# Kernel tuning notes

Hardware: AMD Instinct MI355X
Metric: run time of the kernel (lower is better)

## Reference

```python
import jax, jax.numpy as jnp
import numpy as np

NEG_BIG = -1e12
ALPHA = 0.2  # leaky_relu negative slope


def setup_inputs() -> dict:
    key = jax.random.key(0)
    k1, k2, k3, k4, k5 = jax.random.split(key, 5)
    B, N, C_in, C_out = 8, 2048, 128, 128
    x = jax.random.normal(k1, (B, N, C_in), dtype=jnp.float32)
    adj = jax.random.randint(k2, (B, N, N), 0, 2, dtype=jnp.int32)
    W = jax.random.normal(k3, (C_in, C_out), dtype=jnp.float32)
    a = jax.random.normal(k4, (C_out, 2), dtype=jnp.float32)
    bias = jax.random.normal(k5, (C_out,), dtype=jnp.float32)
    return {"x": x, "adj": adj, "W": W, "a": a, "bias": bias}


def reference(x, adj, W, a, bias):
    # hidden: [B, N, C_out]
    hidden = jnp.matmul(x, W)
    # additive attention components: [B, N, 2] -> attn1, attn2 each [B, N]
    scores = jnp.matmul(hidden, a)
    attn1 = scores[..., 0]
    attn2 = scores[..., 1]
    # outer-sum: [B, N, N]
    attn = attn1[:, :, None] + attn2[:, None, :]
    attn = jnp.where(attn >= 0, attn, ALPHA * attn)  # leaky_relu
    attn = attn + jnp.where(adj > 0, 0.0, NEG_BIG)
    attn = jax.nn.softmax(attn, axis=-1)
    # dropout is identity in eval/reference mode
    out = jnp.matmul(attn, hidden) + bias
    return out
```

## Files before the change

kernel.cpp:

```cpp
#include <hip/hip_runtime.h>
#include <hip/hip_bf16.h>

#define ALPHA 0.2f
#define NEG_BIG -1e12f

constexpr int B_ = 8, N_ = 2048, C_ = 128;
constexpr int IB = 32, JB = 64, NJT = N_ / JB;

typedef __attribute__((ext_vector_type(8))) short short8;
typedef __attribute__((ext_vector_type(8))) unsigned short ushort8;
typedef __attribute__((ext_vector_type(4))) float f32x4;

__device__ __forceinline__ unsigned short f2bf(float f) {
    unsigned int u = __float_as_uint(f);
    u += 0x7fffu + ((u >> 16) & 1u);
    return (unsigned short)(u >> 16);
}

__global__ __launch_bounds__(256) void k1_hidden(
    const float* __restrict__ x, const float* __restrict__ W,
    const float* __restrict__ a, unsigned short* __restrict__ hT,
    float* __restrict__ at1, float* __restrict__ at2)
{
    __shared__ float xs[64][C_];
    __shared__ float Ws[C_][C_];
    const int tid = threadIdx.x;
    const int row0 = blockIdx.x * 64;

    {
        const float4* xsrc = (const float4*)(x + (size_t)row0 * C_);
        float4* xdst = (float4*)&xs[0][0];
        for (int i = tid; i < 64 * C_ / 4; i += 256) xdst[i] = xsrc[i];
        const float4* wsrc = (const float4*)W;
        float4* wdst = (float4*)&Ws[0][0];
        for (int i = tid; i < C_ * C_ / 4; i += 256) wdst[i] = wsrc[i];
    }
    __syncthreads();

    const int tr = tid >> 5, tc = tid & 31;
    const int r0 = tr * 8, c0 = tc * 4;

    float acc[8][4];
#pragma unroll
    for (int i = 0; i < 8; ++i)
#pragma unroll
        for (int j = 0; j < 4; ++j) acc[i][j] = 0.f;

    for (int k = 0; k < C_; k += 4) {
        float4 w0 = *(const float4*)&Ws[k + 0][c0];
        float4 w1 = *(const float4*)&Ws[k + 1][c0];
        float4 w2 = *(const float4*)&Ws[k + 2][c0];
        float4 w3 = *(const float4*)&Ws[k + 3][c0];
#pragma unroll
        for (int rr = 0; rr < 8; ++rr) {
            float4 xv = *(const float4*)&xs[r0 + rr][k];
            acc[rr][0] += xv.x * w0.x + xv.y * w1.x + xv.z * w2.x + xv.w * w3.x;
            acc[rr][1] += xv.x * w0.y + xv.y * w1.y + xv.z * w2.y + xv.w * w3.y;
            acc[rr][2] += xv.x * w0.z + xv.y * w1.z + xv.z * w2.z + xv.w * w3.z;
            acc[rr][3] += xv.x * w0.w + xv.y * w1.w + xv.z * w2.w + xv.w * w3.w;
        }
    }

    float av0[4], av1[4];
#pragma unroll
    for (int cc = 0; cc < 4; ++cc) {
        av0[cc] = a[(c0 + cc) * 2 + 0];
        av1[cc] = a[(c0 + cc) * 2 + 1];
    }
#pragma unroll
    for (int rr = 0; rr < 8; ++rr) {
        float s1 = acc[rr][0] * av0[0] + acc[rr][1] * av0[1] +
                   acc[rr][2] * av0[2] + acc[rr][3] * av0[3];
        float s2 = acc[rr][0] * av1[0] + acc[rr][1] * av1[1] +
                   acc[rr][2] * av1[2] + acc[rr][3] * av1[3];
#pragma unroll
        for (int off = 1; off < 32; off <<= 1) {
            s1 += __shfl_xor(s1, off);
            s2 += __shfl_xor(s2, off);
        }
        if (tc == 0) {
            at1[row0 + r0 + rr] = s1;
            at2[row0 + r0 + rr] = s2;
        }
    }

    const int b = row0 >> 11;
    const int n0 = row0 & (N_ - 1);
#pragma unroll
    for (int cc = 0; cc < 4; ++cc) {
        ushort8 hv;
#pragma unroll
        for (int rr = 0; rr < 8; ++rr) hv[rr] = f2bf(acc[rr][cc]);
        *(ushort8*)(hT + ((size_t)b * C_ + c0 + cc) * N_ + n0 + r0) = hv;
    }
}

__global__ __launch_bounds__(256) void k2_attn(
    const int* __restrict__ adj, const unsigned short* __restrict__ hT,
    const float* __restrict__ at1, const float* __restrict__ at2,
    const float* __restrict__ bias, float* __restrict__ out)
{
    __shared__ unsigned short P[IB][JB + 8];
    __shared__ float mrow[IB], lrow[IB], srow[IB];

    const int tid = threadIdx.x;
    const int b = blockIdx.x >> 6;
    const int i0 = (blockIdx.x & 63) * IB;

    const int r = tid >> 3;
    const int jl = tid & 7;

    if (tid < IB) { mrow[tid] = -3e38f; lrow[tid] = 0.f; }
    __syncthreads();

    const float a1 = at1[(size_t)b * N_ + i0 + r];
    const int* arow = adj + ((size_t)b * N_ + i0 + r) * N_ + jl * 8;
    const float* a2p = at2 + (size_t)b * N_ + jl * 8;

    const int lane = tid & 63;
    const int wv = tid >> 6;
    const int lg = lane >> 4;
    const int ll = lane & 15;
    const unsigned short* hb0 = hT + ((size_t)b * C_ + wv * 32 + ll) * N_;
    const unsigned short* hb1 = hb0 + (size_t)16 * N_;

    f32x4 acc00 = {0.f, 0.f, 0.f, 0.f}, acc01 = {0.f, 0.f, 0.f, 0.f};
    f32x4 acc10 = {0.f, 0.f, 0.f, 0.f}, acc11 = {0.f, 0.f, 0.f, 0.f};

    int4 pf0 = *(const int4*)arow;
    int4 pf1 = *(const int4*)(arow + 4);

    for (int jt = 0; jt < NJT; ++jt) {
        int4 A0 = pf0, A1 = pf1;
        if (jt + 1 < NJT) {
            pf0 = *(const int4*)(arow + (jt + 1) * JB);
            pf1 = *(const int4*)(arow + (jt + 1) * JB + 4);
        }
        float4 f0 = *(const float4*)(a2p + jt * JB);
        float4 f1 = *(const float4*)(a2p + jt * JB + 4);

        float s[8];
        {
            float t;
            t = a1 + f0.x; t = t >= 0.f ? t : ALPHA * t; s[0] = A0.x > 0 ? t : t + NEG_BIG;
            t = a1 + f0.y; t = t >= 0.f ? t : ALPHA * t; s[1] = A0.y > 0 ? t : t + NEG_BIG;
            t = a1 + f0.z; t = t >= 0.f ? t : ALPHA * t; s[2] = A0.z > 0 ? t : t + NEG_BIG;
            t = a1 + f0.w; t = t >= 0.f ? t : ALPHA * t; s[3] = A0.w > 0 ? t : t + NEG_BIG;
            t = a1 + f1.x; t = t >= 0.f ? t : ALPHA * t; s[4] = A1.x > 0 ? t : t + NEG_BIG;
            t = a1 + f1.y; t = t >= 0.f ? t : ALPHA * t; s[5] = A1.y > 0 ? t : t + NEG_BIG;
            t = a1 + f1.z; t = t >= 0.f ? t : ALPHA * t; s[6] = A1.z > 0 ? t : t + NEG_BIG;
            t = a1 + f1.w; t = t >= 0.f ? t : ALPHA * t; s[7] = A1.w > 0 ? t : t + NEG_BIG;
        }
        float tm = s[0];
#pragma unroll
        for (int e = 1; e < 8; ++e) tm = fmaxf(tm, s[e]);
        tm = fmaxf(tm, __shfl_xor(tm, 1));
        tm = fmaxf(tm, __shfl_xor(tm, 2));
        tm = fmaxf(tm, __shfl_xor(tm, 4));

        const float m_old = mrow[r];
        const float m_new = fmaxf(m_old, tm);

        float p[8];
        float ps = 0.f;
#pragma unroll
        for (int e = 0; e < 8; ++e) { p[e] = __expf(s[e] - m_new); ps += p[e]; }
        ps += __shfl_xor(ps, 1);
        ps += __shfl_xor(ps, 2);
        ps += __shfl_xor(ps, 4);

        ushort8 pw;
#pragma unroll
        for (int e = 0; e < 8; ++e) pw[e] = f2bf(p[e]);
        *(ushort8*)&P[r][jl * 8] = pw;

        if (jl == 0) {
            const float sc = __expf(m_old - m_new);
            srow[r] = sc;
            mrow[r] = m_new;
            lrow[r] = lrow[r] * sc + ps;
        }
        __syncthreads();

        const char* Pb = (const char*)P;
        short8 pa0 = *(const short8*)(Pb + ll * 144 + lg * 16);
        short8 pa1 = *(const short8*)(Pb + ll * 144 + lg * 16 + 64);
        short8 pa2 = *(const short8*)(Pb + (ll + 16) * 144 + lg * 16);
        short8 pa3 = *(const short8*)(Pb + (ll + 16) * 144 + lg * 16 + 64);

        const unsigned short* hrow0 = hb0 + jt * JB;
        const unsigned short* hrow1 = hb1 + jt * JB;
        short8 vb00 = *(const short8*)(hrow0 + lg * 8);
        short8 vb01 = *(const short8*)(hrow0 + 32 + lg * 8);
        short8 vb10 = *(const short8*)(hrow1 + lg * 8);
        short8 vb11 = *(const short8*)(hrow1 + 32 + lg * 8);

        float4 sc0 = *(const float4*)&srow[lg * 4];
        float4 sc1 = *(const float4*)&srow[16 + lg * 4];
        acc00[0] *= sc0.x; acc00[1] *= sc0.y; acc00[2] *= sc0.z; acc00[3] *= sc0.w;
        acc01[0] *= sc0.x; acc01[1] *= sc0.y; acc01[2] *= sc0.z; acc01[3] *= sc0.w;
        acc10[0] *= sc1.x; acc10[1] *= sc1.y; acc10[2] *= sc1.z; acc10[3] *= sc1.w;
        acc11[0] *= sc1.x; acc11[1] *= sc1.y; acc11[2] *= sc1.z; acc11[3] *= sc1.w;

        acc00 = __builtin_amdgcn_mfma_f32_16x16x32_bf16(pa0, vb00, acc00, 0, 0, 0);
        acc00 = __builtin_amdgcn_mfma_f32_16x16x32_bf16(pa1, vb01, acc00, 0, 0, 0);
        acc01 = __builtin_amdgcn_mfma_f32_16x16x32_bf16(pa0, vb10, acc01, 0, 0, 0);
        acc01 = __builtin_amdgcn_mfma_f32_16x16x32_bf16(pa1, vb11, acc01, 0, 0, 0);
        acc10 = __builtin_amdgcn_mfma_f32_16x16x32_bf16(pa2, vb00, acc10, 0, 0, 0);
        acc10 = __builtin_amdgcn_mfma_f32_16x16x32_bf16(pa3, vb01, acc10, 0, 0, 0);
        acc11 = __builtin_amdgcn_mfma_f32_16x16x32_bf16(pa2, vb10, acc11, 0, 0, 0);
        acc11 = __builtin_amdgcn_mfma_f32_16x16x32_bf16(pa3, vb11, acc11, 0, 0, 0);

        __syncthreads();
    }

    float4 lw0 = *(const float4*)&lrow[lg * 4];
    float4 lw1 = *(const float4*)&lrow[16 + lg * 4];
    const int c = wv * 32 + ll;
    const float bv0 = bias[c];
    const float bv1 = bias[c + 16];

    float* o0 = out + ((size_t)b * N_ + i0 + lg * 4) * C_ + c;
    o0[0 * C_]      = acc00[0] / lw0.x + bv0;
    o0[1 * C_]      = acc00[1] / lw0.y + bv0;
    o0[2 * C_]      = acc00[2] / lw0.z + bv0;
    o0[3 * C_]      = acc00[3] / lw0.w + bv0;
    o0[0 * C_ + 16] = acc01[0] / lw0.x + bv1;
    o0[1 * C_ + 16] = acc01[1] / lw0.y + bv1;
    o0[2 * C_ + 16] = acc01[2] / lw0.z + bv1;
    o0[3 * C_ + 16] = acc01[3] / lw0.w + bv1;

    float* o1 = o0 + (size_t)16 * C_;
    o1[0 * C_]      = acc10[0] / lw1.x + bv0;
    o1[1 * C_]      = acc10[1] / lw1.y + bv0;
    o1[2 * C_]      = acc10[2] / lw1.z + bv0;
    o1[3 * C_]      = acc10[3] / lw1.w + bv0;
    o1[0 * C_ + 16] = acc11[0] / lw1.x + bv1;
    o1[1 * C_ + 16] = acc11[1] / lw1.y + bv1;
    o1[2 * C_ + 16] = acc11[2] / lw1.z + bv1;
    o1[3 * C_ + 16] = acc11[3] / lw1.w + bv1;
}

extern "C" void kernel_launch(void* const* d_in, const int* in_sizes, int n_in,
                              void* d_out, int out_size, void* d_ws, size_t ws_size,
                              hipStream_t stream) {
    const float* x    = (const float*)d_in[0];
    const int*   adj  = (const int*)d_in[1];
    const float* W    = (const float*)d_in[2];
    const float* a    = (const float*)d_in[3];
    const float* bias = (const float*)d_in[4];
    float* out = (float*)d_out;

    char* ws = (char*)d_ws;
    unsigned short* hT = (unsigned short*)ws;
    float* at1 = (float*)(ws + (size_t)4 * 1024 * 1024);
    float* at2 = (float*)(ws + (size_t)4 * 1024 * 1024 + 64 * 1024);

    k1_hidden<<<(B_ * N_) / 64, 256, 0, stream>>>(x, W, a, hT, at1, at2);
    k2_attn<<<B_ * (N_ / IB), 256, 0, stream>>>(adj, hT, at1, at2, bias, out);
}
```

Before: 85.60 us.

## Retile attention kernel to 16x128 with double-buffered P and LDS-staged at2

Changes the attention tile from 32 rows x 64 columns to 16 rows x 128 columns, so the grid doubles and each block runs half as many j-iterations, with more MFMA work per iteration. The P and srow buffers are double-buffered, which removes the trailing barrier in each iteration. The at2 vector is staged in LDS once per block instead of being read from global memory every iteration, and the float-to-bf16 conversion uses the packed v_cvt_pk_bf16_f32 instruction. The cost is that hT is re-read by twice as many blocks, and the launch bound now requests 4 blocks per CU.

Result: no change. 87.08 us (+1.7%).

```diff
diff --git a/kernel.cpp b/kernel.cpp
--- a/kernel.cpp
+++ b/kernel.cpp
@@ -5,7 +5,7 @@
 #define NEG_BIG -1e12f
 
 constexpr int B_ = 8, N_ = 2048, C_ = 128;
-constexpr int IB = 32, JB = 64, NJT = N_ / JB;
+constexpr int IB = 16, JB = 128, NJT = N_ / JB;
 
 typedef __attribute__((ext_vector_type(8))) short short8;
 typedef __attribute__((ext_vector_type(8))) unsigned short ushort8;
@@ -15,6 +15,12 @@
     unsigned int u = __float_as_uint(f);
     u += 0x7fffu + ((u >> 16) & 1u);
     return (unsigned short)(u >> 16);
+}
+
+__device__ __forceinline__ unsigned int cvtpk_bf16(float lo, float hi) {
+    unsigned int r;
+    asm("v_cvt_pk_bf16_f32 %0, %1, %2" : "=v"(r) : "v"(lo), "v"(hi));
+    return r;
 }
 
 __global__ __launch_bounds__(256) void k1_hidden(
@@ -95,68 +101,84 @@
     }
 }
 
-__global__ __launch_bounds__(256) void k2_attn(
+__global__ __launch_bounds__(256, 4) void k2_attn(
     const int* __restrict__ adj, const unsigned short* __restrict__ hT,
     const float* __restrict__ at1, const float* __restrict__ at2,
     const float* __restrict__ bias, float* __restrict__ out)
 {
-    __shared__ unsigned short P[IB][JB + 8];
-    __shared__ float mrow[IB], lrow[IB], srow[IB];
+    __shared__ unsigned short P[2][IB][JB + 8];
+    __shared__ float at2s[N_];
+    __shared__ float mrow[IB], lrow[IB], srow[2][IB];
 
     const int tid = threadIdx.x;
-    const int b = blockIdx.x >> 6;
-    const int i0 = (blockIdx.x & 63) * IB;
-
-    const int r = tid >> 3;
-    const int jl = tid & 7;
-
+    const int b  = blockIdx.x >> 7;
+    const int i0 = (blockIdx.x & 127) * IB;
+
+    {
+        const float4* src = (const float4*)(at2 + (size_t)b * N_);
+        float4* dst = (float4*)at2s;
+        dst[tid]       = src[tid];
+        dst[tid + 256] = src[tid + 256];
+    }
     if (tid < IB) { mrow[tid] = -3e38f; lrow[tid] = 0.f; }
-    __syncthreads();
-
+
+    const int r  = tid >> 4;
+    const int jl = tid & 15;
     const float a1 = at1[(size_t)b * N_ + i0 + r];
-    const int* arow = adj + ((size_t)b * N_ + i0 + r) * N_ + jl * 8;
-    const float* a2p = at2 + (size_t)b * N_ + jl * 8;
+    const int* arow = adj + ((size_t)(b * N_ + i0 + r)) * N_ + jl * 8;
 
     const int lane = tid & 63;
     const int wv = tid >> 6;
     const int lg = lane >> 4;
     const int ll = lane & 15;
-    const unsigned short* hb0 = hT + ((size_t)b * C_ + wv * 32 + ll) * N_;
-    const unsigned short* hb1 = hb0 + (size_t)16 * N_;
-
-    f32x4 acc00 = {0.f, 0.f, 0.f, 0.f}, acc01 = {0.f, 0.f, 0.f, 0.f};
-    f32x4 acc10 = {0.f, 0.f, 0.f, 0.f}, acc11 = {0.f, 0.f, 0.f, 0.f};
+    const unsigned short* hb = hT + ((size_t)b * C_ + wv * 32 + ll) * N_;
+
+    f32x4 acc0 = {0.f, 0.f, 0.f, 0.f}, acc1 = {0.f, 0.f, 0.f, 0.f};
 
     int4 pf0 = *(const int4*)arow;
     int4 pf1 = *(const int4*)(arow + 4);
 
+    __syncthreads();
+
     for (int jt = 0; jt < NJT; ++jt) {
+        const int buf = jt & 1;
+
+        short8 vb0[4], vb1[4];
+        {
+            const unsigned short* hrow = hb + jt * JB + lg * 8;
+#pragma unroll
+            for (int ks = 0; ks < 4; ++ks) {
+                vb0[ks] = *(const short8*)(hrow + ks * 32);
+                vb1[ks] = *(const short8*)(hrow + (size_t)16 * N_ + ks * 32);
+            }
+        }
+
         int4 A0 = pf0, A1 = pf1;
         if (jt + 1 < NJT) {
             pf0 = *(const int4*)(arow + (jt + 1) * JB);
             pf1 = *(const int4*)(arow + (jt + 1) * JB + 4);
         }
-        float4 f0 = *(const float4*)(a2p + jt * JB);
-        float4 f1 = *(const float4*)(a2p + jt * JB + 4);
+        float4 f0 = *(const float4*)&at2s[jt * JB + jl * 8];
+        float4 f1 = *(const float4*)&at2s[jt * JB + jl * 8 + 4];
 
         float s[8];
         {
             float t;
-            t = a1 + f0.x; t = t >= 0.f ? t : ALPHA * t; s[0] = A0.x > 0 ? t : t + NEG_BIG;
-            t = a1 + f0.y; t = t >= 0.f ? t : ALPHA * t; s[1] = A0.y > 0 ? t : t + NEG_BIG;
-            t = a1 + f0.z; t = t >= 0.f ? t : ALPHA * t; s[2] = A0.z > 0 ? t : t + NEG_BIG;
-            t = a1 + f0.w; t = t >= 0.f ? t : ALPHA * t; s[3] = A0.w > 0 ? t : t + NEG_BIG;
-            t = a1 + f1.x; t = t >= 0.f ? t : ALPHA * t; s[4] = A1.x > 0 ? t : t + NEG_BIG;
-            t = a1 + f1.y; t = t >= 0.f ? t : ALPHA * t; s[5] = A1.y > 0 ? t : t + NEG_BIG;
-            t = a1 + f1.z; t = t >= 0.f ? t : ALPHA * t; s[6] = A1.z > 0 ? t : t + NEG_BIG;
-            t = a1 + f1.w; t = t >= 0.f ? t : ALPHA * t; s[7] = A1.w > 0 ? t : t + NEG_BIG;
-        }
-        float tm = s[0];
-#pragma unroll
-        for (int e = 1; e < 8; ++e) tm = fmaxf(tm, s[e]);
+            t = a1 + f0.x; t = fmaxf(t, ALPHA * t); s[0] = A0.x > 0 ? t : NEG_BIG;
+            t = a1 + f0.y; t = fmaxf(t, ALPHA * t); s[1] = A0.y > 0 ? t : NEG_BIG;
+            t = a1 + f0.z; t = fmaxf(t, ALPHA * t); s[2] = A0.z > 0 ? t : NEG_BIG;
+            t = a1 + f0.w; t = fmaxf(t, ALPHA * t); s[3] = A0.w > 0 ? t : NEG_BIG;
+            t = a1 + f1.x; t = fmaxf(t, ALPHA * t); s[4] = A1.x > 0 ? t : NEG_BIG;
+            t = a1 + f1.y; t = fmaxf(t, ALPHA * t); s[5] = A1.y > 0 ? t : NEG_BIG;
+            t = a1 + f1.z; t = fmaxf(t, ALPHA * t); s[6] = A1.z > 0 ? t : NEG_BIG;
+            t = a1 + f1.w; t = fmaxf(t, ALPHA * t); s[7] = A1.w > 0 ? t : NEG_BIG;
+        }
+        float tm = fmaxf(fmaxf(fmaxf(s[0], s[1]), fmaxf(s[2], s[3])),
+                         fmaxf(fmaxf(s[4], s[5]), fmaxf(s[6], s[7])));
         tm = fmaxf(tm, __shfl_xor(tm, 1));
         tm = fmaxf(tm, __shfl_xor(tm, 2));
         tm = fmaxf(tm, __shfl_xor(tm, 4));
+        tm = fmaxf(tm, __shfl_xor(tm, 8));
 
         const float m_old = mrow[r];
         const float m_new = fmaxf(m_old, tm);
@@ -168,77 +190,54 @@
         ps += __shfl_xor(ps, 1);
         ps += __shfl_xor(ps, 2);
         ps += __shfl_xor(ps, 4);
-
-        ushort8 pw;
-#pragma unroll
-        for (int e = 0; e < 8; ++e) pw[e] = f2bf(p[e]);
-        *(ushort8*)&P[r][jl * 8] = pw;
+        ps += __shfl_xor(ps, 8);
+
+        int4 pw;
+        pw.x = (int)cvtpk_bf16(p[0], p[1]);
+        pw.y = (int)cvtpk_bf16(p[2], p[3]);
+        pw.z = (int)cvtpk_bf16(p[4], p[5]);
+        pw.w = (int)cvtpk_bf16(p[6], p[7]);
+        *(int4*)&P[buf][r][jl * 8] = pw;
 
         if (jl == 0) {
             const float sc = __expf(m_old - m_new);
-            srow[r] = sc;
+            srow[buf][r] = sc;
             mrow[r] = m_new;
             lrow[r] = lrow[r] * sc + ps;
         }
         __syncthreads();
 
-        const char* Pb = (const char*)P;
-        short8 pa0 = *(const short8*)(Pb + ll * 144 + lg * 16);
-        short8 pa1 = *(const short8*)(Pb + ll * 144 + lg * 16 + 64);
-        short8 pa2 = *(const short8*)(Pb + (ll + 16) * 144 + lg * 16);
-        short8 pa3 = *(const short8*)(Pb + (ll + 16) * 144 + lg * 16 + 64);
-
-        const unsigned short* hrow0 = hb0 + jt * JB;
-        const unsigned short* hrow1 = hb1 + jt * JB;
-        short8 vb00 = *(const short8*)(hrow0 + lg * 8);
-        short8 vb01 = *(const short8*)(hrow0 + 32 + lg * 8);
-        short8 vb10 = *(const short8*)(hrow1 + lg * 8);
-        short8 vb11 = *(const short8*)(hrow1 + 32 + lg * 8);
-
-        float4 sc0 = *(const float4*)&srow[lg * 4];
-        float4 sc1 = *(const float4*)&srow[16 + lg * 4];
-        acc00[0] *= sc0.x; acc00[1] *= sc0.y; acc00[2] *= sc0.z; acc00[3] *= sc0.w;
-        acc01[0] *= sc0.x; acc01[1] *= sc0.y; acc01[2] *= sc0.z; acc01[3] *= sc0.w;
-        acc10[0] *= sc1.x; acc10[1] *= sc1.y; acc10[2] *= sc1.z; acc10[3] *= sc1.w;
-        acc11[0] *= sc1.x; acc11[1] *= sc1.y; acc11[2] *= sc1.z; acc11[3] *= sc1.w;
-
-        acc00 = __builtin_amdgcn_mfma_f32_16x16x32_bf16(pa0, vb00, acc00, 0, 0, 0);
-        acc00 = __builtin_amdgcn_mfma_f32_16x16x32_bf16(pa1, vb01, acc00, 0, 0, 0);
-        acc01 = __builtin_amdgcn_mfma_f32_16x16x32_bf16(pa0, vb10, acc01, 0, 0, 0);
-        acc01 = __builtin_amdgcn_mfma_f32_16x16x32_bf16(pa1, vb11, acc01, 0, 0, 0);
-        acc10 = __builtin_amdgcn_mfma_f32_16x16x32_bf16(pa2, vb00, acc10, 0, 0, 0);
-        acc10 = __builtin_amdgcn_mfma_f32_16x16x32_bf16(pa3, vb01, acc10, 0, 0, 0);
-        acc11 = __builtin_amdgcn_mfma_f32_16x16x32_bf16(pa2, vb10, acc11, 0, 0, 0);
-        acc11 = __builtin_amdgcn_mfma_f32_16x16x32_bf16(pa3, vb11, acc11, 0, 0, 0);
-
-        __syncthreads();
-    }
-
-    float4 lw0 = *(const float4*)&lrow[lg * 4];
-    float4 lw1 = *(const float4*)&lrow[16 + lg * 4];
+        const char* Pb = (const char*)P[buf];
+        short8 pa[4];
+#pragma unroll
+        for (int ks = 0; ks < 4; ++ks)
+            pa[ks] = *(const short8*)(Pb + ll * 272 + ks * 64 + lg * 16);
+
+        float4 sc4 = *(const float4*)&srow[buf][lg * 4];
+        acc0[0] *= sc4.x; acc0[1] *= sc4.y; acc0[2] *= sc4.z; acc0[3] *= sc4.w;
+        acc1[0] *= sc4.x; acc1[1] *= sc4.y; acc1[2] *= sc4.z; acc1[3] *= sc4.w;
+
+#pragma unroll
+        for (int ks = 0; ks < 4; ++ks) {
+            acc0 = __builtin_amdgcn_mfma_f32_16x16x32_bf16(pa[ks], vb0[ks], acc0, 0, 0, 0);
+            acc1 = __builtin_amdgcn_mfma_f32_16x16x32_bf16(pa[ks], vb1[ks], acc1, 0, 0, 0);
+        }
+    }
+
+    float4 lw = *(const float4*)&lrow[lg * 4];
     const int c = wv * 32 + ll;
     const float bv0 = bias[c];
     const float bv1 = bias[c + 16];
 
-    float* o0 = out + ((size_t)b * N_ + i0 + lg * 4) * C_ + c;
-    o0[0 * C_]      = acc00[0] / lw0.x + bv0;
-    o0[1 * C_]      = acc00[1] / lw0.y + bv0;
-    o0[2 * C_]      = acc00[2] / lw0.z + bv0;
-    o0[3 * C_]      = acc00[3] / lw0.w + bv0;
-    o0[0 * C_ + 16] = acc01[0] / lw0.x + bv1;
-    o0[1 * C_ + 16] = acc01[1] / lw0.y + bv1;
-    o0[2 * C_ + 16] = acc01[2] / lw0.z + bv1;
-    o0[3 * C_ + 16] = acc01[3] / lw0.w + bv1;
-
-    float* o1 = o0 + (size_t)16 * C_;
-    o1[0 * C_]      = acc10[0] / lw1.x + bv0;
-    o1[1 * C_]      = acc10[1] / lw1.y + bv0;
-    o1[2 * C_]      = acc10[2] / lw1.z + bv0;
-    o1[3 * C_]      = acc10[3] / lw1.w + bv0;
-    o1[0 * C_ + 16] = acc11[0] / lw1.x + bv1;
-    o1[1 * C_ + 16] = acc11[1] / lw1.y + bv1;
-    o1[2 * C_ + 16] = acc11[2] / lw1.z + bv1;
-    o1[3 * C_ + 16] = acc11[3] / lw1.w + bv1;
+    float* o = out + ((size_t)(b * N_ + i0 + lg * 4)) * C_ + c;
+    o[0 * C_]      = acc0[0] / lw.x + bv0;
+    o[1 * C_]      = acc0[1] / lw.y + bv0;
+    o[2 * C_]      = acc0[2] / lw.z + bv0;
+    o[3 * C_]      = acc0[3] / lw.w + bv0;
+    o[0 * C_ + 16] = acc1[0] / lw.x + bv1;
+    o[1 * C_ + 16] = acc1[1] / lw.y + bv1;
+    o[2 * C_ + 16] = acc1[2] / lw.z + bv1;
+    o[3 * C_ + 16] = acc1[3] / lw.w + bv1;
 }
 
 extern "C" void kernel_launch(void* const* d_in, const int* in_sizes, int n_in,
```
